# Kernel tuning notes

Hardware: AMD Instinct MI355X
Metric: run time of the kernel (lower is better)

Reference implementation:

```python
import jax, jax.numpy as jnp
import numpy as np

G, A, HID, NF, L = 512, 32, 256, 11, 4
EMB = HID - 1  # embed_dim = in_node_nf - 1 (condition_time)


def _forward(node_feat, pos, t,
             enc_w1, enc_b1, enc_w2, enc_b2,
             ew1, eb1, ew2, eb2,
             xw1, xb1, xw2, xb2,
             hw1, hb1, hw2, hb2,
             rg1, rgb1, rv1, rvb1, rg2, rgb2, rv2, rvb2, rw3, rb3,
             batch, edge_src, edge_dst):
    silu = jax.nn.silu
    N = node_feat.shape[0]
    # remove_mean_batch: subtract per-graph centroid (scatter_mean)
    cnt = jax.ops.segment_sum(jnp.ones((N, 1), pos.dtype), batch, num_segments=G)
    mean = jax.ops.segment_sum(pos, batch, num_segments=G) / cnt
    x0 = pos - mean[batch]
    # fragment encoder MLP (last layer no activation): 11 -> 22 -> 255
    h = silu(node_feat @ enc_w1 + enc_b1) @ enc_w2 + enc_b2
    # condition on time (t scalar broadcast to all nodes)
    h = jnp.concatenate([h, jnp.full((N, 1), t[0], h.dtype)], axis=1)  # [N, 256]
    x = x0
    for l in range(L):  # EGNN message-passing layers
        hi, hj = h[edge_src], h[edge_dst]
        rel = x[edge_src] - x[edge_dst]                    # [E, 3]
        d2 = jnp.sum(rel * rel, axis=-1, keepdims=True)    # [E, 1]
        e_in = jnp.concatenate([hi, hj, d2], axis=1)       # [E, 2*HID+1]
        m = silu(silu(e_in @ ew1[l] + eb1[l]) @ ew2[l] + eb2[l])  # edge MLP phi_e
        agg = jax.ops.segment_sum(m, edge_src, num_segments=N)
        coef = silu(m @ xw1[l] + xb1[l]) @ xw2[l] + xb2[l]        # phi_x -> [E,1]
        # subgraph_mask is all ones (single fragment), coord update equivariant
        x = x + jax.ops.segment_sum(rel * coef, edge_src, num_segments=N)
        h = h + silu(jnp.concatenate([h, agg], axis=1) @ hw1[l] + hb1[l]) @ hw2[l] + hb2[l]
    # GatedMLP readout: 256 -> 256 -> 256 -> 1, last layer plain linear
    g = silu(h @ rg1 + rgb1) * (h @ rv1 + rvb1)
    g = silu(g @ rg2 + rgb2) * (g @ rv2 + rvb2)
    y = g @ rw3 + rb3                                      # [N, 1]
    ae = jax.ops.segment_sum(y, batch, num_segments=G)[:, 0]  # per-graph energy
    forces = x - x0                                        # equivariant coord displacement
    return ae, forces


def setup_inputs() -> dict:
    key = jax.random.key(0)
    kc = [0]
    def nk():
        kc[0] += 1
        return jax.random.fold_in(key, kc[0])
    N = G * A
    node_feat = jax.random.normal(nk(), (N, NF), jnp.float32)
    pos = jax.random.normal(nk(), (N, 3), jnp.float32) * 3.0
    batch = jnp.repeat(jnp.arange(G), A)
    # fully-connected intra-graph edges without self loops (get_edges_index)
    i = np.arange(A)
    s, d = np.meshgrid(i, i, indexing='ij')
    msk = s != d
    s, d = s[msk], d[msk]
    offs = (np.arange(G) * A)[:, None]
    edge_src = jnp.asarray((s[None, :] + offs).reshape(-1))
    edge_dst = jnp.asarray((d[None, :] + offs).reshape(-1))
    def lin(fi, fo):
        return jax.random.normal(nk(), (fi, fo), jnp.float32) / np.sqrt(fi)
    def linL(fi, fo):
        return jax.random.normal(nk(), (L, fi, fo), jnp.float32) / np.sqrt(fi)
    inp = dict(node_feat=node_feat, pos=pos, t=jnp.zeros((1,), jnp.float32),
               enc_w1=lin(NF, 2 * NF), enc_b1=jnp.zeros((2 * NF,), jnp.float32),
               enc_w2=lin(2 * NF, EMB), enc_b2=jnp.zeros((EMB,), jnp.float32),
               ew1=linL(2 * HID + 1, HID), eb1=jnp.zeros((L, HID), jnp.float32),
               ew2=linL(HID, HID), eb2=jnp.zeros((L, HID), jnp.float32),
               xw1=linL(HID, HID), xb1=jnp.zeros((L, HID), jnp.float32),
               xw2=linL(HID, 1) * 0.1, xb2=jnp.zeros((L, 1), jnp.float32),
               hw1=linL(2 * HID, HID), hb1=jnp.zeros((L, HID), jnp.float32),
               hw2=linL(HID, HID), hb2=jnp.zeros((L, HID), jnp.float32),
               rg1=lin(HID, HID), rgb1=jnp.zeros((HID,), jnp.float32),
               rv1=lin(HID, HID), rvb1=jnp.zeros((HID,), jnp.float32),
               rg2=lin(HID, HID), rgb2=jnp.zeros((HID,), jnp.float32),
               rv2=lin(HID, HID), rvb2=jnp.zeros((HID,), jnp.float32),
               rw3=lin(HID, 1), rb3=jnp.zeros((1,), jnp.float32),
               batch=batch, edge_src=edge_src, edge_dst=edge_dst)
    return inp


def reference(node_feat, pos, t,
              enc_w1, enc_b1, enc_w2, enc_b2,
              ew1, eb1, ew2, eb2,
              xw1, xb1, xw2, xb2,
              hw1, hb1, hw2, hb2,
              rg1, rgb1, rv1, rvb1, rg2, rgb2, rv2, rvb2, rw3, rb3,
              batch, edge_src, edge_dst):
    return _forward(node_feat, pos, t,
                    enc_w1, enc_b1, enc_w2, enc_b2,
                    ew1, eb1, ew2, eb2,
                    xw1, xb1, xw2, xb2,
                    hw1, hb1, hw2, hb2,
                    rg1, rgb1, rv1, rvb1, rg2, rgb2, rv2, rvb2, rw3, rb3,
                    batch, edge_src, edge_dst)
```

## Files before the change

kernel.cpp:

```cpp
#include <hip/hip_runtime.h>

#define NGRAPH 512
#define NA 32
#define HID 256
#define NT 512
#define NLAYER 4

using short8 = __attribute__((ext_vector_type(8))) short;
using f32x4  = __attribute__((ext_vector_type(4))) float;

#define MFMA(a,b,c)  __builtin_amdgcn_mfma_f32_16x16x32_bf16((a),(b),(c),0,0,0)
#define MFMA8(a,b,c) __builtin_amdgcn_mfma_f32_16x16x32_fp8_fp8((a),(b),(c),0,0,0)

__device__ __forceinline__ float CL(float x) {
    return fminf(fmaxf(x, -1e15f), 1e15f);
}
__device__ __forceinline__ float CL8(float x) {
    return fminf(fmaxf(x, -240.f), 240.f);
}
__device__ __forceinline__ float silu_f(float x) {
    return x / (1.0f + __expf(-x));
}
__device__ __forceinline__ unsigned short bf16t(float x) {
    return (unsigned short)(__float_as_uint(x) >> 16);
}
__device__ __forceinline__ float up16(unsigned short u) {
    return __uint_as_float(((unsigned)u) << 16);
}
__device__ __forceinline__ long pk8(const float* v) {
    int lo = __builtin_amdgcn_cvt_pk_fp8_f32(v[0], v[1], 0, false);
    lo     = __builtin_amdgcn_cvt_pk_fp8_f32(v[2], v[3], lo, true);
    int hi = __builtin_amdgcn_cvt_pk_fp8_f32(v[4], v[5], 0, false);
    hi     = __builtin_amdgcn_cvt_pk_fp8_f32(v[6], v[7], hi, true);
    return ((long)(unsigned)lo) | (((long)hi) << 32);
}
__device__ __forceinline__ unsigned char fp8b(float v) {
    return (unsigned char)(__builtin_amdgcn_cvt_pk_fp8_f32(v, v, 0, false) & 0xff);
}
__device__ __forceinline__ int swzi(int row, int col) {
    return row*256 + (col ^ ((row & 7) << 3));
}
__device__ __forceinline__ short8 ldA(const unsigned short* sA, int row, int kk, int sg) {
    return *(const short8*)(sA + row*256 + ((kk*32 + sg*8) ^ ((row & 7) << 3)));
}
__device__ __forceinline__ long ldA8(const unsigned char* sA, int row, int kk, int sg) {
    return *(const long*)(sA + row*256 + ((kk*32 + sg*8) ^ ((row & 7) << 3)));
}
__device__ __forceinline__ short8 ldBfrag(const float* __restrict__ W,
                                          int kk, int nt, int li, int sg) {
    const float* p = W + (size_t)(kk*32 + sg*8)*HID + nt*16 + li;
    short8 r;
#pragma unroll
    for (int e = 0; e < 8; ++e) r[e] = (short)bf16t(p[(size_t)e*HID]);
    return r;
}
__device__ __forceinline__ long ldBfrag8(const float* __restrict__ W,
                                         int kk, int nt, int li, int sg) {
    const float* p = W + (size_t)(kk*32 + sg*8)*HID + nt*16 + li;
    float v[8];
#pragma unroll
    for (int e = 0; e < 8; ++e) v[e] = CL8(p[(size_t)e*HID]);
    return pk8(v);
}

extern "C" __global__ void __launch_bounds__(NT)
egnn_mfma(const float* __restrict__ node_feat, const float* __restrict__ pos,
          const float* __restrict__ tt,
          const float* __restrict__ enc_w1, const float* __restrict__ enc_b1,
          const float* __restrict__ enc_w2, const float* __restrict__ enc_b2,
          const float* __restrict__ ew1, const float* __restrict__ eb1,
          const float* __restrict__ ew2, const float* __restrict__ eb2,
          const float* __restrict__ xw1, const float* __restrict__ xb1,
          const float* __restrict__ xw2, const float* __restrict__ xb2,
          const float* __restrict__ hw1, const float* __restrict__ hb1,
          const float* __restrict__ hw2, const float* __restrict__ hb2,
          const float* __restrict__ rg1, const float* __restrict__ rgb1,
          const float* __restrict__ rv1, const float* __restrict__ rvb1,
          const float* __restrict__ rg2, const float* __restrict__ rgb2,
          const float* __restrict__ rv2, const float* __restrict__ rvb2,
          const float* __restrict__ rw3, const float* __restrict__ rb3,
          float* __restrict__ out)
{
    __shared__ unsigned short sHb [NA*HID];
    __shared__ unsigned short sPa [NA*HID];
    __shared__ unsigned short sPb [NA*HID];
    __shared__ unsigned short sAgg[NA*HID];
    __shared__ long sPoolL[4096];
    __shared__ float sD2[NA*NA];
    __shared__ float sW1d[HID], sB1[HID];
    __shared__ float sh_x[NA*3], sh_x0[NA*3], sh_dx[NA*3];
    __shared__ float sh_coef[2][64];
    __shared__ float sh_a1[NA*22];
    __shared__ float sh_red[8];

    unsigned char* sAb = (unsigned char*)sPoolL;
    unsigned char* sYm = (unsigned char*)sPoolL + 16384;
    float*         sF  = (float*)sPoolL;

    const int g    = blockIdx.x;
    const int tid  = threadIdx.x;
    const int w    = tid >> 6;
    const int lane = tid & 63;
    const int li   = lane & 15;
    const int sg   = lane >> 4;
    const int nb   = g * NA;

    if (tid < NA) {
        float px = pos[(nb+tid)*3+0], py = pos[(nb+tid)*3+1], pz = pos[(nb+tid)*3+2];
        float sx = px, sy = py, sz = pz;
#pragma unroll
        for (int mm = 1; mm < 32; mm <<= 1) {
            sx += __shfl_xor(sx, mm); sy += __shfl_xor(sy, mm); sz += __shfl_xor(sz, mm);
        }
        const float inv = 1.0f/32.0f;
        const float xx = px - sx*inv, xy = py - sy*inv, xz = pz - sz*inv;
        sh_x [tid*3+0]=xx; sh_x [tid*3+1]=xy; sh_x [tid*3+2]=xz;
        sh_x0[tid*3+0]=xx; sh_x0[tid*3+1]=xy; sh_x0[tid*3+2]=xz;
        sh_dx[tid*3+0]=0.f; sh_dx[tid*3+1]=0.f; sh_dx[tid*3+2]=0.f;
    }

    for (int e = tid; e < NA*22; e += NT) {
        const int node = e / 22, u = e - node*22;
        const float* nfp = node_feat + (size_t)(nb+node)*11;
        float s = enc_b1[u];
#pragma unroll
        for (int f = 0; f < 11; ++f) s = fmaf(nfp[f], enc_w1[f*22+u], s);
        sh_a1[e] = CL(silu_f(s));
    }
    __syncthreads();
    for (int e = tid; e < NA*255; e += NT) {
        const int node = e / 255, o = e - node*255;
        const float* ap = sh_a1 + node*22;
        float s = enc_b2[o];
#pragma unroll
        for (int u = 0; u < 22; ++u) s = fmaf(ap[u], enc_w2[u*255+o], s);
        sHb[swzi(node, o)] = bf16t(CL(s));
    }
    if (tid < NA) sHb[swzi(tid, 255)] = bf16t(tt[0]);
    __syncthreads();

    for (int l = 0; l < NLAYER; ++l) {
        const float* W1   = ew1 + (size_t)l*513*HID;
        const float* b1v  = eb1 + l*HID;
        const float* W2   = ew2 + (size_t)l*HID*HID;
        const float* b2v  = eb2 + l*HID;
        const float* XW1  = xw1 + (size_t)l*HID*HID;
        const float* xb1v = xb1 + l*HID;
        const float* XW2  = xw2 + (size_t)l*HID;
        const float  xb2v = xb2[l];
        const float* HW1  = hw1 + (size_t)l*2*HID*HID;
        const float* hb1v = hb1 + l*HID;
        const float* HW2  = hw2 + (size_t)l*HID*HID;
        const float* hb2v = hb2 + l*HID;

        for (int e = tid; e < NA*NA; e += NT) {
            const int i = e >> 5, j = e & 31;
            const float rx = sh_x[i*3+0]-sh_x[j*3+0];
            const float ry = sh_x[i*3+1]-sh_x[j*3+1];
            const float rz = sh_x[i*3+2]-sh_x[j*3+2];
            sD2[e] = rx*rx + ry*ry + rz*rz;
        }
        if (tid < HID) { sW1d[tid] = W1[512*HID + tid]; sB1[tid] = b1v[tid]; }

        {
            const int m = w >> 2, s = w & 3;
            const float* Wm = W1 + (size_t)m*256*HID;
            f32x4 acc[2][4] = {};
#pragma unroll
            for (int kk = 0; kk < 8; ++kk) {
                const short8 a0 = ldA(sHb, li,      kk, sg);
                const short8 a1_= ldA(sHb, 16 + li, kk, sg);
#pragma unroll
                for (int q = 0; q < 4; ++q) {
                    const short8 b = ldBfrag(Wm, kk, s*4+q, li, sg);
                    acc[0][q] = MFMA(a0,  b, acc[0][q]);
                    acc[1][q] = MFMA(a1_, b, acc[1][q]);
                }
            }
            unsigned short* dst = m ? sPb : sPa;
#pragma unroll
            for (int mt = 0; mt < 2; ++mt)
#pragma unroll
                for (int q = 0; q < 4; ++q)
#pragma unroll
                    for (int r = 0; r < 4; ++r) {
                        const int row = mt*16 + sg*4 + r;
                        const int col = (s*4+q)*16 + li;
                        dst[swzi(row, col)] = bf16t(CL(acc[mt][q][r]));
                    }
        }
        long w2f8[16], x1f8[16];
#pragma unroll
        for (int kk = 0; kk < 8; ++kk)
#pragma unroll
            for (int q = 0; q < 2; ++q) {
                w2f8[kk*2+q] = ldBfrag8(W2,  kk, w*2+q, li, sg);
                x1f8[kk*2+q] = ldBfrag8(XW1, kk, w*2+q, li, sg);
            }
        const float b2c[2] = { b2v[(w*2+0)*16+li],  b2v[(w*2+1)*16+li]  };
        const float xbc[2] = { xb1v[(w*2+0)*16+li], xb1v[(w*2+1)*16+li] };
        const float xwc[2] = { XW2[(w*2+0)*16+li],  XW2[(w*2+1)*16+li]  };
        __syncthreads();

        int par = 0;
        for (int pair = 0; pair < 16; ++pair, par ^= 1) {
            const int i0 = pair*2;
            if (tid < 64) sh_coef[par][tid] = 0.f;
            {
                const int c = tid & 31, rg = tid >> 5;
                const float4* wp = (const float4*)(sW1d + c*8);
                const float4* bp = (const float4*)(sB1 + c*8);
                const float4 w0 = wp[0], w1 = wp[1], bq0 = bp[0], bq1 = bp[1];
                const float wd[8] = {w0.x,w0.y,w0.z,w0.w,w1.x,w1.y,w1.z,w1.w};
                const float bb[8] = {bq0.x,bq0.y,bq0.z,bq0.w,bq1.x,bq1.y,bq1.z,bq1.w};
                const short8 paA = *(const short8*)(sPa + (i0+0)*256 + ((c*8) ^ (((i0+0)&7)<<3)));
                const short8 paB = *(const short8*)(sPa + (i0+1)*256 + ((c*8) ^ (((i0+1)&7)<<3)));
                float pab0[8], pab1[8];
#pragma unroll
                for (int e = 0; e < 8; ++e) {
                    pab0[e] = up16((unsigned short)paA[e]) + bb[e];
                    pab1[e] = up16((unsigned short)paB[e]) + bb[e];
                }
#pragma unroll
                for (int k = 0; k < 4; ++k) {
                    const int row = rg + 16*k;
                    const int j   = rg + 16*(k & 1);
                    const float d2v = sD2[(i0 + (k>>1))*32 + j];
                    const short8 pb8 = *(const short8*)(sPb + j*256 + ((c*8) ^ ((j&7)<<3)));
                    float f[8];
#pragma unroll
                    for (int e = 0; e < 8; ++e) {
                        const float base = (k>>1) ? pab1[e] : pab0[e];
                        f[e] = CL8(silu_f(base + up16((unsigned short)pb8[e]) + d2v*wd[e]));
                    }
                    *(long*)(sAb + row*256 + ((c*8) ^ ((row&7)<<3))) = pk8(f);
                }
            }
            __syncthreads();

            f32x4 a1[4][2] = {};
#pragma unroll
            for (int kk = 0; kk < 8; ++kk)
#pragma unroll
                for (int mt = 0; mt < 4; ++mt) {
                    const long a = ldA8(sAb, mt*16 + li, kk, sg);
                    a1[mt][0] = MFMA8(a, w2f8[kk*2+0], a1[mt][0]);
                    a1[mt][1] = MFMA8(a, w2f8[kk*2+1], a1[mt][1]);
                }
#pragma unroll
            for (int q = 0; q < 2; ++q)
#pragma unroll
                for (int mt = 0; mt < 4; ++mt)
#pragma unroll
                    for (int r = 0; r < 4; ++r)
                        a1[mt][q][r] = CL8(silu_f(a1[mt][q][r] + b2c[q]));
#pragma unroll
            for (int ip = 0; ip < 2; ++ip) {
                const int ig = i0 + ip;
                const int drow = ip*32 + ig;
#pragma unroll
                for (int q = 0; q < 2; ++q) {
                    float s = 0.f;
#pragma unroll
                    for (int mt2 = 0; mt2 < 2; ++mt2) {
                        const int mt = ip*2 + mt2;
#pragma unroll
                        for (int r = 0; r < 4; ++r) {
                            const int row = mt*16 + sg*4 + r;
                            s += (row == drow) ? 0.f : a1[mt][q][r];
                        }
                    }
                    s += __shfl_xor(s, 16);
                    s += __shfl_xor(s, 32);
                    if (lane < 16)
                        sAgg[swzi(ig, (w*2+q)*16 + lane)] = bf16t(CL(s));
                }
            }
#pragma unroll
            for (int q = 0; q < 2; ++q)
#pragma unroll
                for (int mt = 0; mt < 4; ++mt)
#pragma unroll
                    for (int r = 0; r < 4; ++r) {
                        const int row = mt*16 + sg*4 + r;
                        const int col = (w*2+q)*16 + li;
                        sYm[row*256 + (col ^ ((row&7)<<3))] = fp8b(a1[mt][q][r]);
                    }
            __syncthreads();

            f32x4 a2[4][2] = {};
#pragma unroll
            for (int kk = 0; kk < 8; ++kk)
#pragma unroll
                for (int mt = 0; mt < 4; ++mt) {
                    const long a = ldA8(sYm, mt*16 + li, kk, sg);
                    a2[mt][0] = MFMA8(a, x1f8[kk*2+0], a2[mt][0]);
                    a2[mt][1] = MFMA8(a, x1f8[kk*2+1], a2[mt][1]);
                }
#pragma unroll
            for (int mt = 0; mt < 4; ++mt) {
#pragma unroll
                for (int r = 0; r < 4; ++r) {
                    float v = silu_f(a2[mt][0][r] + xbc[0]) * xwc[0]
                            + silu_f(a2[mt][1][r] + xbc[1]) * xwc[1];
                    v += __shfl_xor(v, 1); v += __shfl_xor(v, 2);
                    v += __shfl_xor(v, 4); v += __shfl_xor(v, 8);
                    if (li == 0) atomicAdd(&sh_coef[par][mt*16 + sg*4 + r], CL(v));
                }
            }
            __syncthreads();

            if (tid < 64) {
                const int ip = tid >> 5, j = tid & 31, ig = i0 + ip;
                const float cf = CL(sh_coef[par][tid] + xb2v);
                const float rx = sh_x[ig*3+0]-sh_x[j*3+0];
                const float ry = sh_x[ig*3+1]-sh_x[j*3+1];
                const float rz = sh_x[ig*3+2]-sh_x[j*3+2];
                const bool diag = (j == ig);
                float vx = diag ? 0.f : rx*cf;
                float vy = diag ? 0.f : ry*cf;
                float vz = diag ? 0.f : rz*cf;
#pragma unroll
                for (int mm = 1; mm < 32; mm <<= 1) {
                    vx += __shfl_xor(vx, mm); vy += __shfl_xor(vy, mm); vz += __shfl_xor(vz, mm);
                }
                if ((tid & 31) == 0) {
                    sh_dx[ig*3+0] = CL(sh_dx[ig*3+0] + vx);
                    sh_dx[ig*3+1] = CL(sh_dx[ig*3+1] + vy);
                    sh_dx[ig*3+2] = CL(sh_dx[ig*3+2] + vz);
                }
            }
        }
        __syncthreads();

        if (tid < NA*3) { sh_x[tid] = CL(sh_x[tid] + sh_dx[tid]); sh_dx[tid] = 0.f; }

        {
            const int kh = w >> 2, s = w & 3;
            const unsigned short* Amat = kh ? sAgg : sHb;
            const float* Bmat = HW1 + (size_t)kh*256*HID;
            f32x4 acc[2][4] = {};
#pragma unroll
            for (int kk = 0; kk < 8; ++kk) {
                const short8 a0 = ldA(Amat, li,      kk, sg);
                const short8 a1_= ldA(Amat, 16 + li, kk, sg);
#pragma unroll
                for (int q = 0; q < 4; ++q) {
                    const short8 b = ldBfrag(Bmat, kk, s*4+q, li, sg);
                    acc[0][q] = MFMA(a0,  b, acc[0][q]);
                    acc[1][q] = MFMA(a1_, b, acc[1][q]);
                }
            }
            if (kh == 0) {
#pragma unroll
                for (int mt = 0; mt < 2; ++mt)
#pragma unroll
                    for (int q = 0; q < 4; ++q)
#pragma unroll
                        for (int r = 0; r < 4; ++r)
                            sF[(mt*16+sg*4+r)*256 + (s*4+q)*16 + li] = acc[mt][q][r];
            }
            __syncthreads();
            if (kh == 1) {
#pragma unroll
                for (int mt = 0; mt < 2; ++mt)
#pragma unroll
                    for (int q = 0; q < 4; ++q)
#pragma unroll
                        for (int r = 0; r < 4; ++r) {
                            const int row = mt*16+sg*4+r, col = (s*4+q)*16+li;
                            const float u = CL(silu_f(sF[row*256+col] + acc[mt][q][r] + hb1v[col]));
                            sPa[swzi(row, col)] = bf16t(u);
                        }
            }
        }
        __syncthreads();
        {
            const int kh = w >> 2, s = w & 3;
            f32x4 acc[2][4] = {};
#pragma unroll
            for (int kk4 = 0; kk4 < 4; ++kk4) {
                const int kk = kh*4 + kk4;
                const short8 a0 = ldA(sPa, li,      kk, sg);
                const short8 a1_= ldA(sPa, 16 + li, kk, sg);
#pragma unroll
                for (int q = 0; q < 4; ++q) {
                    const short8 b = ldBfrag(HW2, kk, s*4+q, li, sg);
                    acc[0][q] = MFMA(a0,  b, acc[0][q]);
                    acc[1][q] = MFMA(a1_, b, acc[1][q]);
                }
            }
            if (kh == 0) {
#pragma unroll
                for (int mt = 0; mt < 2; ++mt)
#pragma unroll
                    for (int q = 0; q < 4; ++q)
#pragma unroll
                        for (int r = 0; r < 4; ++r)
                            sF[(mt*16+sg*4+r)*256 + (s*4+q)*16 + li] = acc[mt][q][r];
            }
            __syncthreads();
            if (kh == 1) {
#pragma unroll
                for (int mt = 0; mt < 2; ++mt)
#pragma unroll
                    for (int q = 0; q < 4; ++q)
#pragma unroll
                        for (int r = 0; r < 4; ++r) {
                            const int row = mt*16+sg*4+r, col = (s*4+q)*16+li;
                            const int idx = swzi(row, col);
                            sHb[idx] = bf16t(CL(up16(sHb[idx]) + sF[row*256+col]
                                                + acc[mt][q][r] + hb2v[col]));
                        }
            }
        }
        __syncthreads();
    }

    {
        const int mrole = w >> 2, s = w & 3;
        {
            const float* G = mrole ? rv1 : rg1;
            f32x4 acc[2][4] = {};
#pragma unroll
            for (int kk = 0; kk < 8; ++kk) {
                const short8 a0 = ldA(sHb, li,      kk, sg);
                const short8 a1_= ldA(sHb, 16 + li, kk, sg);
#pragma unroll
                for (int q = 0; q < 4; ++q) {
                    const short8 b = ldBfrag(G, kk, s*4+q, li, sg);
                    acc[0][q] = MFMA(a0,  b, acc[0][q]);
                    acc[1][q] = MFMA(a1_, b, acc[1][q]);
                }
            }
            if (mrole == 0) {
#pragma unroll
                for (int mt = 0; mt < 2; ++mt)
#pragma unroll
                    for (int q = 0; q < 4; ++q)
#pragma unroll
                        for (int r = 0; r < 4; ++r)
                            sF[(mt*16+sg*4+r)*256 + (s*4+q)*16 + li] = acc[mt][q][r];
            }
            __syncthreads();
            if (mrole == 1) {
#pragma unroll
                for (int mt = 0; mt < 2; ++mt)
#pragma unroll
                    for (int q = 0; q < 4; ++q)
#pragma unroll
                        for (int r = 0; r < 4; ++r) {
                            const int row = mt*16+sg*4+r, col = (s*4+q)*16+li;
                            const float v = CL(silu_f(sF[row*256+col] + rgb1[col])
                                               * (acc[mt][q][r] + rvb1[col]));
                            sPb[swzi(row, col)] = bf16t(v);
                        }
            }
        }
        __syncthreads();
        {
            const float* G = mrole ? rv2 : rg2;
            f32x4 acc[2][4] = {};
#pragma unroll
            for (int kk = 0; kk < 8; ++kk) {
                const short8 a0 = ldA(sPb, li,      kk, sg);
                const short8 a1_= ldA(sPb, 16 + li, kk, sg);
#pragma unroll
                for (int q = 0; q < 4; ++q) {
                    const short8 b = ldBfrag(G, kk, s*4+q, li, sg);
                    acc[0][q] = MFMA(a0,  b, acc[0][q]);
                    acc[1][q] = MFMA(a1_, b, acc[1][q]);
                }
            }
            if (mrole == 0) {
#pragma unroll
                for (int mt = 0; mt < 2; ++mt)
#pragma unroll
                    for (int q = 0; q < 4; ++q)
#pragma unroll
                        for (int r = 0; r < 4; ++r)
                            sF[(mt*16+sg*4+r)*256 + (s*4+q)*16 + li] = acc[mt][q][r];
            }
            __syncthreads();
            if (mrole == 1) {
                float p = 0.f;
#pragma unroll
                for (int mt = 0; mt < 2; ++mt)
#pragma unroll
                    for (int q = 0; q < 4; ++q)
#pragma unroll
                        for (int r = 0; r < 4; ++r) {
                            const int row = mt*16+sg*4+r, col = (s*4+q)*16+li;
                            p += CL(silu_f(sF[row*256+col] + rgb2[col])
                                    * (acc[mt][q][r] + rvb2[col])) * rw3[col];
                        }
                p = CL(p);
#pragma unroll
                for (int mm = 1; mm < 64; mm <<= 1) p += __shfl_xor(p, mm);
                if (lane == 0) sh_red[w] = p;
            }
        }
        __syncthreads();
        if (tid == 0) {
            float s = sh_red[4] + sh_red[5] + sh_red[6] + sh_red[7];
            out[g] = s + (float)NA * rb3[0];
        }
    }
    if (tid < NA*3) out[NGRAPH + g*(NA*3) + tid] = sh_x[tid] - sh_x0[tid];
}

extern "C" __global__ void egnn_node_pad1() {}
extern "C" __global__ void egnn_node_pad2() {}

extern "C" void kernel_launch(void* const* d_in, const int* in_sizes, int n_in,
                              void* d_out, int out_size, void* d_ws, size_t ws_size,
                              hipStream_t stream)
{
    const float* node_feat = (const float*)d_in[0];
    const float* pos    = (const float*)d_in[1];
    const float* tt     = (const float*)d_in[2];
    const float* enc_w1 = (const float*)d_in[3];
    const float* enc_b1 = (const float*)d_in[4];
    const float* enc_w2 = (const float*)d_in[5];
    const float* enc_b2 = (const float*)d_in[6];
    const float* ew1    = (const float*)d_in[7];
    const float* eb1    = (const float*)d_in[8];
    const float* ew2    = (const float*)d_in[9];
    const float* eb2    = (const float*)d_in[10];
    const float* xw1    = (const float*)d_in[11];
    const float* xb1    = (const float*)d_in[12];
    const float* xw2    = (const float*)d_in[13];
    const float* xb2    = (const float*)d_in[14];
    const float* hw1    = (const float*)d_in[15];
    const float* hb1    = (const float*)d_in[16];
    const float* hw2    = (const float*)d_in[17];
    const float* hb2    = (const float*)d_in[18];
    const float* rg1    = (const float*)d_in[19];
    const float* rgb1   = (const float*)d_in[20];
    const float* rv1    = (const float*)d_in[21];
    const float* rvb1   = (const float*)d_in[22];
    const float* rg2    = (const float*)d_in[23];
    const float* rgb2   = (const float*)d_in[24];
    const float* rv2    = (const float*)d_in[25];
    const float* rvb2   = (const float*)d_in[26];
    const float* rw3    = (const float*)d_in[27];
    const float* rb3    = (const float*)d_in[28];
    (void)d_ws; (void)ws_size; (void)in_sizes; (void)n_in;

    egnn_mfma<<<NGRAPH, NT, 0, stream>>>(
        node_feat, pos, tt, enc_w1, enc_b1, enc_w2, enc_b2,
        ew1, eb1, ew2, eb2, xw1, xb1, xw2, xb2,
        hw1, hb1, hw2, hb2, rg1, rgb1, rv1, rvb1,
        rg2, rgb2, rv2, rvb2, rw3, rb3,
        (float*)d_out);
    egnn_node_pad1<<<1, 64, 0, stream>>>();
    egnn_node_pad2<<<1, 64, 0, stream>>>();
}
```

Baseline: 2.217 ms.

## Cut registers and LDS to fit more blocks per CU, restructure GEMM warp splits

Sets launch bounds to ask for 4 blocks per CU. Shrinks LDS by storing the aggregate in fp8, packing the d2-weight and bias pairs as bf16 into one word, and reusing a single fp8 buffer for the edge activations. GEMMs now loop over one output tile at a time to cut live accumulators. The node-update and readout GEMMs change from a K-split or role-split across warps with an LDS fp32 reduction to an M/N split, which removes the sF scratch and a barrier. The aggregate half of the node-update GEMM now uses fp8 MFMA, which lowers precision and risks accuracy, and the tighter register budget may cause spills.

```diff
diff --git a/kernel.cpp b/kernel.cpp
--- a/kernel.cpp
+++ b/kernel.cpp
@@ -12,15 +12,9 @@
 #define MFMA(a,b,c)  __builtin_amdgcn_mfma_f32_16x16x32_bf16((a),(b),(c),0,0,0)
 #define MFMA8(a,b,c) __builtin_amdgcn_mfma_f32_16x16x32_fp8_fp8((a),(b),(c),0,0,0)
 
-__device__ __forceinline__ float CL(float x) {
-    return fminf(fmaxf(x, -1e15f), 1e15f);
-}
-__device__ __forceinline__ float CL8(float x) {
-    return fminf(fmaxf(x, -240.f), 240.f);
-}
-__device__ __forceinline__ float silu_f(float x) {
-    return x / (1.0f + __expf(-x));
-}
+__device__ __forceinline__ float CL(float x)  { return fminf(fmaxf(x, -1e15f), 1e15f); }
+__device__ __forceinline__ float CL8(float x) { return fminf(fmaxf(x, -240.f), 240.f); }
+__device__ __forceinline__ float silu_f(float x) { return x / (1.0f + __expf(-x)); }
 __device__ __forceinline__ unsigned short bf16t(float x) {
     return (unsigned short)(__float_as_uint(x) >> 16);
 }
@@ -34,6 +28,11 @@
     hi     = __builtin_amdgcn_cvt_pk_fp8_f32(v[6], v[7], hi, true);
     return ((long)(unsigned)lo) | (((long)hi) << 32);
 }
+__device__ __forceinline__ unsigned pk4(float a, float b, float c, float d) {
+    int v = __builtin_amdgcn_cvt_pk_fp8_f32(a, b, 0, false);
+    v     = __builtin_amdgcn_cvt_pk_fp8_f32(c, d, v, true);
+    return (unsigned)v;
+}
 __device__ __forceinline__ unsigned char fp8b(float v) {
     return (unsigned char)(__builtin_amdgcn_cvt_pk_fp8_f32(v, v, 0, false) & 0xff);
 }
@@ -63,7 +62,7 @@
     return pk8(v);
 }
 
-extern "C" __global__ void __launch_bounds__(NT)
+extern "C" __global__ void __launch_bounds__(NT, 4)
 egnn_mfma(const float* __restrict__ node_feat, const float* __restrict__ pos,
           const float* __restrict__ tt,
           const float* __restrict__ enc_w1, const float* __restrict__ enc_b1,
@@ -84,18 +83,15 @@
     __shared__ unsigned short sHb [NA*HID];
     __shared__ unsigned short sPa [NA*HID];
     __shared__ unsigned short sPb [NA*HID];
-    __shared__ unsigned short sAgg[NA*HID];
-    __shared__ long sPoolL[4096];
+    __shared__ unsigned char  sAgg[NA*HID];
+    __shared__ unsigned char  sAbm[2*NA*HID];
     __shared__ float sD2[NA*NA];
-    __shared__ float sW1d[HID], sB1[HID];
+    __shared__ unsigned sWB[HID];
     __shared__ float sh_x[NA*3], sh_x0[NA*3], sh_dx[NA*3];
     __shared__ float sh_coef[2][64];
-    __shared__ float sh_a1[NA*22];
     __shared__ float sh_red[8];
 
-    unsigned char* sAb = (unsigned char*)sPoolL;
-    unsigned char* sYm = (unsigned char*)sPoolL + 16384;
-    float*         sF  = (float*)sPoolL;
+    float* sA1 = (float*)sAbm;
 
     const int g    = blockIdx.x;
     const int tid  = threadIdx.x;
@@ -125,12 +121,12 @@
         float s = enc_b1[u];
 #pragma unroll
         for (int f = 0; f < 11; ++f) s = fmaf(nfp[f], enc_w1[f*22+u], s);
-        sh_a1[e] = CL(silu_f(s));
+        sA1[e] = CL(silu_f(s));
     }
     __syncthreads();
     for (int e = tid; e < NA*255; e += NT) {
         const int node = e / 255, o = e - node*255;
-        const float* ap = sh_a1 + node*22;
+        const float* ap = sA1 + node*22;
         float s = enc_b2[o];
 #pragma unroll
         for (int u = 0; u < 22; ++u) s = fmaf(ap[u], enc_w2[u*255+o], s);
@@ -148,7 +144,8 @@
         const float* xb1v = xb1 + l*HID;
         const float* XW2  = xw2 + (size_t)l*HID;
         const float  xb2v = xb2[l];
-        const float* HW1  = hw1 + (size_t)l*2*HID*HID;
+        const float* HW1a = hw1 + (size_t)l*2*HID*HID;
+        const float* HW1b = HW1a + 256*HID;
         const float* hb1v = hb1 + l*HID;
         const float* HW2  = hw2 + (size_t)l*HID*HID;
         const float* hb2v = hb2 + l*HID;
@@ -160,34 +157,29 @@
             const float rz = sh_x[i*3+2]-sh_x[j*3+2];
             sD2[e] = rx*rx + ry*ry + rz*rz;
         }
-        if (tid < HID) { sW1d[tid] = W1[512*HID + tid]; sB1[tid] = b1v[tid]; }
+        if (tid < HID)
+            sWB[tid] = (unsigned)bf16t(W1[512*HID + tid]) | ((unsigned)bf16t(b1v[tid]) << 16);
 
         {
             const int m = w >> 2, s = w & 3;
             const float* Wm = W1 + (size_t)m*256*HID;
-            f32x4 acc[2][4] = {};
-#pragma unroll
-            for (int kk = 0; kk < 8; ++kk) {
-                const short8 a0 = ldA(sHb, li,      kk, sg);
-                const short8 a1_= ldA(sHb, 16 + li, kk, sg);
-#pragma unroll
-                for (int q = 0; q < 4; ++q) {
-                    const short8 b = ldBfrag(Wm, kk, s*4+q, li, sg);
-                    acc[0][q] = MFMA(a0,  b, acc[0][q]);
-                    acc[1][q] = MFMA(a1_, b, acc[1][q]);
-                }
-            }
             unsigned short* dst = m ? sPb : sPa;
 #pragma unroll
-            for (int mt = 0; mt < 2; ++mt)
+            for (int mt = 0; mt < 2; ++mt) {
+                f32x4 acc[4] = {};
+#pragma unroll
+                for (int kk = 0; kk < 8; ++kk) {
+                    const short8 a = ldA(sHb, mt*16 + li, kk, sg);
+#pragma unroll
+                    for (int q = 0; q < 4; ++q)
+                        acc[q] = MFMA(a, ldBfrag(Wm, kk, s*4+q, li, sg), acc[q]);
+                }
 #pragma unroll
                 for (int q = 0; q < 4; ++q)
 #pragma unroll
-                    for (int r = 0; r < 4; ++r) {
-                        const int row = mt*16 + sg*4 + r;
-                        const int col = (s*4+q)*16 + li;
-                        dst[swzi(row, col)] = bf16t(CL(acc[mt][q][r]));
-                    }
+                    for (int r = 0; r < 4; ++r)
+                        dst[swzi(mt*16 + sg*4 + r, (s*4+q)*16 + li)] = bf16t(CL(acc[q][r]));
+            }
         }
         long w2f8[16], x1f8[16];
 #pragma unroll
@@ -208,11 +200,13 @@
             if (tid < 64) sh_coef[par][tid] = 0.f;
             {
                 const int c = tid & 31, rg = tid >> 5;
-                const float4* wp = (const float4*)(sW1d + c*8);
-                const float4* bp = (const float4*)(sB1 + c*8);
-                const float4 w0 = wp[0], w1 = wp[1], bq0 = bp[0], bq1 = bp[1];
-                const float wd[8] = {w0.x,w0.y,w0.z,w0.w,w1.x,w1.y,w1.z,w1.w};
-                const float bb[8] = {bq0.x,bq0.y,bq0.z,bq0.w,bq1.x,bq1.y,bq1.z,bq1.w};
+                float wd[8], bb[8];
+#pragma unroll
+                for (int e = 0; e < 8; ++e) {
+                    const unsigned u = sWB[c*8 + e];
+                    wd[e] = up16((unsigned short)(u & 0xffff));
+                    bb[e] = up16((unsigned short)(u >> 16));
+                }
                 const short8 paA = *(const short8*)(sPa + (i0+0)*256 + ((c*8) ^ (((i0+0)&7)<<3)));
                 const short8 paB = *(const short8*)(sPa + (i0+1)*256 + ((c*8) ^ (((i0+1)&7)<<3)));
                 float pab0[8], pab1[8];
@@ -233,33 +227,30 @@
                         const float base = (k>>1) ? pab1[e] : pab0[e];
                         f[e] = CL8(silu_f(base + up16((unsigned short)pb8[e]) + d2v*wd[e]));
                     }
-                    *(long*)(sAb + row*256 + ((c*8) ^ ((row&7)<<3))) = pk8(f);
+                    *(long*)(sAbm + row*256 + ((c*8) ^ ((row&7)<<3))) = pk8(f);
                 }
             }
             __syncthreads();
 
-            f32x4 a1[4][2] = {};
-#pragma unroll
-            for (int kk = 0; kk < 8; ++kk)
-#pragma unroll
-                for (int mt = 0; mt < 4; ++mt) {
-                    const long a = ldA8(sAb, mt*16 + li, kk, sg);
-                    a1[mt][0] = MFMA8(a, w2f8[kk*2+0], a1[mt][0]);
-                    a1[mt][1] = MFMA8(a, w2f8[kk*2+1], a1[mt][1]);
-                }
-#pragma unroll
-            for (int q = 0; q < 2; ++q)
+            unsigned mheld[2][4];
+#pragma unroll
+            for (int q = 0; q < 2; ++q) {
+                f32x4 acc[4] = {};
+#pragma unroll
+                for (int kk = 0; kk < 8; ++kk)
+#pragma unroll
+                    for (int mt = 0; mt < 4; ++mt)
+                        acc[mt] = MFMA8(ldA8(sAbm, mt*16 + li, kk, sg),
+                                        w2f8[kk*2+q], acc[mt]);
 #pragma unroll
                 for (int mt = 0; mt < 4; ++mt)
 #pragma unroll
                     for (int r = 0; r < 4; ++r)
-                        a1[mt][q][r] = CL8(silu_f(a1[mt][q][r] + b2c[q]));
-#pragma unroll
-            for (int ip = 0; ip < 2; ++ip) {
-                const int ig = i0 + ip;
-                const int drow = ip*32 + ig;
-#pragma unroll
-                for (int q = 0; q < 2; ++q) {
+                        acc[mt][r] = CL8(silu_f(acc[mt][r] + b2c[q]));
+#pragma unroll
+                for (int ip = 0; ip < 2; ++ip) {
+                    const int ig = i0 + ip;
+                    const int drow = ip*32 + ig;
                     float s = 0.f;
 #pragma unroll
                     for (int mt2 = 0; mt2 < 2; ++mt2) {
@@ -267,46 +258,53 @@
 #pragma unroll
                         for (int r = 0; r < 4; ++r) {
                             const int row = mt*16 + sg*4 + r;
-                            s += (row == drow) ? 0.f : a1[mt][q][r];
+                            s += (row == drow) ? 0.f : acc[mt][r];
                         }
                     }
                     s += __shfl_xor(s, 16);
                     s += __shfl_xor(s, 32);
-                    if (lane < 16)
-                        sAgg[swzi(ig, (w*2+q)*16 + lane)] = bf16t(CL(s));
-                }
-            }
+                    if (lane < 16) {
+                        const int col = (w*2+q)*16 + lane;
+                        sAgg[ig*256 + (col ^ ((ig & 7) << 3))] = fp8b(CL8(s));
+                    }
+                }
+#pragma unroll
+                for (int mt = 0; mt < 4; ++mt)
+                    mheld[q][mt] = pk4(acc[mt][0], acc[mt][1], acc[mt][2], acc[mt][3]);
+            }
+            __syncthreads();
 #pragma unroll
             for (int q = 0; q < 2; ++q)
 #pragma unroll
-                for (int mt = 0; mt < 4; ++mt)
+                for (int mt = 0; mt < 4; ++mt) {
+                    const unsigned mv = mheld[q][mt];
 #pragma unroll
                     for (int r = 0; r < 4; ++r) {
                         const int row = mt*16 + sg*4 + r;
                         const int col = (w*2+q)*16 + li;
-                        sYm[row*256 + (col ^ ((row&7)<<3))] = fp8b(a1[mt][q][r]);
+                        sAbm[row*256 + (col ^ ((row&7)<<3))] = (unsigned char)(mv >> (8*r));
                     }
+                }
             __syncthreads();
 
-            f32x4 a2[4][2] = {};
-#pragma unroll
-            for (int kk = 0; kk < 8; ++kk)
-#pragma unroll
-                for (int mt = 0; mt < 4; ++mt) {
-                    const long a = ldA8(sYm, mt*16 + li, kk, sg);
-                    a2[mt][0] = MFMA8(a, x1f8[kk*2+0], a2[mt][0]);
-                    a2[mt][1] = MFMA8(a, x1f8[kk*2+1], a2[mt][1]);
-                }
-#pragma unroll
-            for (int mt = 0; mt < 4; ++mt) {
-#pragma unroll
-                for (int r = 0; r < 4; ++r) {
-                    float v = silu_f(a2[mt][0][r] + xbc[0]) * xwc[0]
-                            + silu_f(a2[mt][1][r] + xbc[1]) * xwc[1];
-                    v += __shfl_xor(v, 1); v += __shfl_xor(v, 2);
-                    v += __shfl_xor(v, 4); v += __shfl_xor(v, 8);
-                    if (li == 0) atomicAdd(&sh_coef[par][mt*16 + sg*4 + r], CL(v));
-                }
+#pragma unroll
+            for (int q = 0; q < 2; ++q) {
+                f32x4 acc[4] = {};
+#pragma unroll
+                for (int kk = 0; kk < 8; ++kk)
+#pragma unroll
+                    for (int mt = 0; mt < 4; ++mt)
+                        acc[mt] = MFMA8(ldA8(sAbm, mt*16 + li, kk, sg),
+                                        x1f8[kk*2+q], acc[mt]);
+#pragma unroll
+                for (int mt = 0; mt < 4; ++mt)
+#pragma unroll
+                    for (int r = 0; r < 4; ++r) {
+                        float v = silu_f(acc[mt][r] + xbc[q]) * xwc[q];
+                        v += __shfl_xor(v, 1); v += __shfl_xor(v, 2);
+                        v += __shfl_xor(v, 4); v += __shfl_xor(v, 8);
+                        if (li == 0) atomicAdd(&sh_coef[par][mt*16 + sg*4 + r], CL(v));
+                    }
             }
             __syncthreads();
 
@@ -336,173 +334,90 @@
         if (tid < NA*3) { sh_x[tid] = CL(sh_x[tid] + sh_dx[tid]); sh_dx[tid] = 0.f; }
 
         {
-            const int kh = w >> 2, s = w & 3;
-            const unsigned short* Amat = kh ? sAgg : sHb;
-            const float* Bmat = HW1 + (size_t)kh*256*HID;
-            f32x4 acc[2][4] = {};
+            const int mg = w >> 2, ng = w & 3;
+#pragma unroll
+            for (int q = 0; q < 4; ++q) {
+                f32x4 acc = {};
+#pragma unroll
+                for (int kk = 0; kk < 8; ++kk) {
+                    acc = MFMA (ldA (sHb,  mg*16 + li, kk, sg),
+                                ldBfrag (HW1a, kk, ng*4+q, li, sg), acc);
+                    acc = MFMA8(ldA8(sAgg, mg*16 + li, kk, sg),
+                                ldBfrag8(HW1b, kk, ng*4+q, li, sg), acc);
+                }
+                const int col = (ng*4+q)*16 + li;
+                const float bc = hb1v[col];
+#pragma unroll
+                for (int r = 0; r < 4; ++r)
+                    sPa[swzi(mg*16 + sg*4 + r, col)] = bf16t(CL(silu_f(acc[r] + bc)));
+            }
+        }
+        __syncthreads();
+        {
+            const int mg = w >> 2, ng = w & 3;
+#pragma unroll
+            for (int q = 0; q < 4; ++q) {
+                f32x4 acc = {};
+#pragma unroll
+                for (int kk = 0; kk < 8; ++kk)
+                    acc = MFMA(ldA(sPa, mg*16 + li, kk, sg),
+                               ldBfrag(HW2, kk, ng*4+q, li, sg), acc);
+                const int col = (ng*4+q)*16 + li;
+                const float bc = hb2v[col];
+#pragma unroll
+                for (int r = 0; r < 4; ++r) {
+                    const int idx = swzi(mg*16 + sg*4 + r, col);
+                    sHb[idx] = bf16t(CL(up16(sHb[idx]) + acc[r] + bc));
+                }
+            }
+        }
+        __syncthreads();
+    }
+
+    {
+        const int mg = w >> 2, ng = w & 3;
+#pragma unroll
+        for (int q = 0; q < 4; ++q) {
+            f32x4 ag = {}, av = {};
 #pragma unroll
             for (int kk = 0; kk < 8; ++kk) {
-                const short8 a0 = ldA(Amat, li,      kk, sg);
-                const short8 a1_= ldA(Amat, 16 + li, kk, sg);
-#pragma unroll
-                for (int q = 0; q < 4; ++q) {
-                    const short8 b = ldBfrag(Bmat, kk, s*4+q, li, sg);
-                    acc[0][q] = MFMA(a0,  b, acc[0][q]);
-                    acc[1][q] = MFMA(a1_, b, acc[1][q]);
-                }
-            }
-            if (kh == 0) {
-#pragma unroll
-                for (int mt = 0; mt < 2; ++mt)
-#pragma unroll
-                    for (int q = 0; q < 4; ++q)
-#pragma unroll
-                        for (int r = 0; r < 4; ++r)
-                            sF[(mt*16+sg*4+r)*256 + (s*4+q)*16 + li] = acc[mt][q][r];
-            }
-            __syncthreads();
-            if (kh == 1) {
-#pragma unroll
-                for (int mt = 0; mt < 2; ++mt)
-#pragma unroll
-                    for (int q = 0; q < 4; ++q)
-#pragma unroll
-                        for (int r = 0; r < 4; ++r) {
-                            const int row = mt*16+sg*4+r, col = (s*4+q)*16+li;
-                            const float u = CL(silu_f(sF[row*256+col] + acc[mt][q][r] + hb1v[col]));
-                            sPa[swzi(row, col)] = bf16t(u);
-                        }
-            }
-        }
-        __syncthreads();
-        {
-            const int kh = w >> 2, s = w & 3;
-            f32x4 acc[2][4] = {};
-#pragma unroll
-            for (int kk4 = 0; kk4 < 4; ++kk4) {
-                const int kk = kh*4 + kk4;
-                const short8 a0 = ldA(sPa, li,      kk, sg);
-                const short8 a1_= ldA(sPa, 16 + li, kk, sg);
-#pragma unroll
-                for (int q = 0; q < 4; ++q) {
-                    const short8 b = ldBfrag(HW2, kk, s*4+q, li, sg);
-                    acc[0][q] = MFMA(a0,  b, acc[0][q]);
-                    acc[1][q] = MFMA(a1_, b, acc[1][q]);
-                }
-            }
-            if (kh == 0) {
-#pragma unroll
-                for (int mt = 0; mt < 2; ++mt)
-#pragma unroll
-                    for (int q = 0; q < 4; ++q)
-#pragma unroll
-                        for (int r = 0; r < 4; ++r)
-                            sF[(mt*16+sg*4+r)*256 + (s*4+q)*16 + li] = acc[mt][q][r];
-            }
-            __syncthreads();
-            if (kh == 1) {
-#pragma unroll
-                for (int mt = 0; mt < 2; ++mt)
-#pragma unroll
-                    for (int q = 0; q < 4; ++q)
-#pragma unroll
-                        for (int r = 0; r < 4; ++r) {
-                            const int row = mt*16+sg*4+r, col = (s*4+q)*16+li;
-                            const int idx = swzi(row, col);
-                            sHb[idx] = bf16t(CL(up16(sHb[idx]) + sF[row*256+col]
-                                                + acc[mt][q][r] + hb2v[col]));
-                        }
-            }
-        }
-        __syncthreads();
-    }
-
-    {
-        const int mrole = w >> 2, s = w & 3;
-        {
-            const float* G = mrole ? rv1 : rg1;
-            f32x4 acc[2][4] = {};
+                const short8 a = ldA(sHb, mg*16 + li, kk, sg);
+                ag = MFMA(a, ldBfrag(rg1, kk, ng*4+q, li, sg), ag);
+                av = MFMA(a, ldBfrag(rv1, kk, ng*4+q, li, sg), av);
+            }
+            const int col = (ng*4+q)*16 + li;
+            const float bg = rgb1[col], bv = rvb1[col];
+#pragma unroll
+            for (int r = 0; r < 4; ++r)
+                sPb[swzi(mg*16 + sg*4 + r, col)] =
+                    bf16t(CL(silu_f(ag[r] + bg) * (av[r] + bv)));
+        }
+        __syncthreads();
+        float p = 0.f;
+#pragma unroll
+        for (int q = 0; q < 4; ++q) {
+            f32x4 ag = {}, av = {};
 #pragma unroll
             for (int kk = 0; kk < 8; ++kk) {
-                const short8 a0 = ldA(sHb, li,      kk, sg);
-                const short8 a1_= ldA(sHb, 16 + li, kk, sg);
-#pragma unroll
-                for (int q = 0; q < 4; ++q) {
-                    const short8 b = ldBfrag(G, kk, s*4+q, li, sg);
-                    acc[0][q] = MFMA(a0,  b, acc[0][q]);
-                    acc[1][q] = MFMA(a1_, b, acc[1][q]);
-                }
-            }
-            if (mrole == 0) {
-#pragma unroll
-                for (int mt = 0; mt < 2; ++mt)
-#pragma unroll
-                    for (int q = 0; q < 4; ++q)
-#pragma unroll
-                        for (int r = 0; r < 4; ++r)
-                            sF[(mt*16+sg*4+r)*256 + (s*4+q)*16 + li] = acc[mt][q][r];
-            }
-            __syncthreads();
-            if (mrole == 1) {
-#pragma unroll
-                for (int mt = 0; mt < 2; ++mt)
-#pragma unroll
-                    for (int q = 0; q < 4; ++q)
-#pragma unroll
-                        for (int r = 0; r < 4; ++r) {
-                            const int row = mt*16+sg*4+r, col = (s*4+q)*16+li;
-                            const float v = CL(silu_f(sF[row*256+col] + rgb1[col])
-                                               * (acc[mt][q][r] + rvb1[col]));
-                            sPb[swzi(row, col)] = bf16t(v);
-                        }
-            }
-        }
-        __syncthreads();
-        {
-            const float* G = mrole ? rv2 : rg2;
-            f32x4 acc[2][4] = {};
-#pragma unroll
-            for (int kk = 0; kk < 8; ++kk) {
-                const short8 a0 = ldA(sPb, li,      kk, sg);
-                const short8 a1_= ldA(sPb, 16 + li, kk, sg);
-#pragma unroll
-                for (int q = 0; q < 4; ++q) {
-                    const short8 b = ldBfrag(G, kk, s*4+q, li, sg);
-                    acc[0][q] = MFMA(a0,  b, acc[0][q]);
-                    acc[1][q] = MFMA(a1_, b, acc[1][q]);
-                }
-            }
-            if (mrole == 0) {
-#pragma unroll
-                for (int mt = 0; mt < 2; ++mt)
-#pragma unroll
-                    for (int q = 0; q < 4; ++q)
-#pragma unroll
-                        for (int r = 0; r < 4; ++r)
-                            sF[(mt*16+sg*4+r)*256 + (s*4+q)*16 + li] = acc[mt][q][r];
-            }
-            __syncthreads();
-            if (mrole == 1) {
-                float p = 0.f;
-#pragma unroll
-                for (int mt = 0; mt < 2; ++mt)
-#pragma unroll
-                    for (int q = 0; q < 4; ++q)
-#pragma unroll
-                        for (int r = 0; r < 4; ++r) {
-                            const int row = mt*16+sg*4+r, col = (s*4+q)*16+li;
-                            p += CL(silu_f(sF[row*256+col] + rgb2[col])
-                                    * (acc[mt][q][r] + rvb2[col])) * rw3[col];
-                        }
-                p = CL(p);
-#pragma unroll
-                for (int mm = 1; mm < 64; mm <<= 1) p += __shfl_xor(p, mm);
-                if (lane == 0) sh_red[w] = p;
-            }
-        }
+                const short8 a = ldA(sPb, mg*16 + li, kk, sg);
+                ag = MFMA(a, ldBfrag(rg2, kk, ng*4+q, li, sg), ag);
+                av = MFMA(a, ldBfrag(rv2, kk, ng*4+q, li, sg), av);
+            }
+            const int col = (ng*4+q)*16 + li;
+            const float bg = rgb2[col], bv = rvb2[col], rw = rw3[col];
+#pragma unroll
+            for (int r = 0; r < 4; ++r)
+                p += CL(silu_f(ag[r] + bg) * (av[r] + bv)) * rw;
+        }
+        p = CL(p);
+#pragma unroll
+        for (int mm = 1; mm < 64; mm <<= 1) p += __shfl_xor(p, mm);
+        if (lane == 0) sh_red[w] = p;
         __syncthreads();
         if (tid == 0) {
-            float s = sh_red[4] + sh_red[5] + sh_red[6] + sh_red[7];
+            float s = 0.f;
+#pragma unroll
+            for (int ww = 0; ww < 8; ++ww) s += sh_red[ww];
             out[g] = s + (float)NA * rb3[0];
         }
     }
```

After: 2.983 ms. 34.5% more time.
